# Performance work log

Measured on AMD Instinct MI355X. Metric: run time of the kernel, lower is better.

Reference implementation:

```python
import jax, jax.numpy as jnp
import numpy as np

DEPTH = 128
NEG_MAX = -jnp.finfo(jnp.float32).max


def setup_inputs() -> dict:
    key = jax.random.key(0)
    ks = jax.random.split(key, 10)
    B, S, F, C = 16, 2048, 512, 1000
    x = jax.random.normal(ks[0], (B, S, F), dtype=jnp.float32)
    attention_mask = jax.random.randint(ks[1], (B, S, S), 0, 2) == 1
    s = 1.0 / np.sqrt(F)
    Wq = jax.random.uniform(ks[2], (F, DEPTH), jnp.float32, -s, s)
    bq = jax.random.uniform(ks[3], (DEPTH,), jnp.float32, -s, s)
    Wk = jax.random.uniform(ks[4], (F, DEPTH), jnp.float32, -s, s)
    bk = jax.random.uniform(ks[5], (DEPTH,), jnp.float32, -s, s)
    Wv = jax.random.uniform(ks[6], (F, DEPTH), jnp.float32, -s, s)
    bv = jax.random.uniform(ks[7], (DEPTH,), jnp.float32, -s, s)
    sl = 1.0 / np.sqrt(DEPTH)
    Wl = jax.random.uniform(ks[8], (DEPTH, C), jnp.float32, -sl, sl)
    bl = jax.random.uniform(ks[9], (C,), jnp.float32, -sl, sl)
    return {"x": x, "attention_mask": attention_mask,
            "Wq": Wq, "bq": bq, "Wk": Wk, "bk": bk,
            "Wv": Wv, "bv": bv, "Wl": Wl, "bl": bl}


def reference(x, attention_mask, Wq, bq, Wk, bk, Wv, bv, Wl, bl):
    # x: [B, S, F]; single-head attention with depth=128
    q = (x @ Wq + bq) * (DEPTH ** -0.5)          # [B, S, D] (is_scaled_dot_product)
    k = x @ Wk + bk                               # [B, S, D]
    v = x @ Wv + bv                               # [B, S, D]
    logit = jnp.einsum('bsd,btd->bst', q, k)      # [B, S, S]
    # masked_fill_(mask, -float_max) then added to logits
    logit = logit + jnp.where(attention_mask, NEG_MAX, 0.0)
    attn = jax.nn.softmax(logit, axis=2)
    out = jnp.einsum('bst,btd->bsd', attn, v)     # [B, S, D]
    out = out @ Wl + bl                           # [B, S, C]
    return out.mean(axis=1)                       # [B, C]
```

## Files before the change

kernel.cpp:

```cpp
#include <hip/hip_runtime.h>
#include <stdint.h>

#define BB 16
#define SS 2048
#define FF 512
#define DD 128
#define CC 1000

typedef __attribute__((ext_vector_type(8))) short bf16x8;
typedef __attribute__((ext_vector_type(4))) float f32x4;

__device__ __forceinline__ unsigned short f2bf(float f) {
  unsigned x;
  __builtin_memcpy(&x, &f, 4);
  x = x + 0x7FFFu + ((x >> 16) & 1u);
  return (unsigned short)(x >> 16);
}
__device__ __forceinline__ float bf2f(unsigned short u) {
  unsigned x = ((unsigned)u) << 16;
  float f;
  __builtin_memcpy(&f, &x, 4);
  return f;
}
__device__ __forceinline__ unsigned pk2(float a, float b) {
  return (unsigned)f2bf(a) | ((unsigned)f2bf(b) << 16);
}

#define WS_PK   0
#define WS_Q    8388608
#define WS_K    16777216
#define WS_V    25165824
#define WS_WT   33554432
#define WS_WGP  33947648
#define WS_END  42336256

__global__ __launch_bounds__(256) void k_prep(const void* __restrict__ mask,
                                              const float* __restrict__ Wq,
                                              const float* __restrict__ Wk,
                                              const float* __restrict__ Wv,
                                              unsigned short* __restrict__ wt,
                                              unsigned* __restrict__ pk) {
  __shared__ unsigned red;
  const int tid = threadIdx.x;
  if (tid == 0) red = 0;
  __syncthreads();
  {
    unsigned a = 0;
    const unsigned* m32 = (const unsigned*)mask;
#pragma unroll
    for (int j = 0; j < 4; ++j) a |= m32[tid * 4 + j] & 0xFFFFFF00u;
    if (a) atomicOr(&red, 1u);
  }
  __syncthreads();
  const bool isInt = (red == 0);

  const long long base = (long long)blockIdx.x * 32768;
  for (int it = 0; it < 128; ++it) {
    long long e = base + it * 256 + tid;
    int val;
    if (isInt) val = ((const int*)mask)[e];
    else       val = ((const unsigned char*)mask)[e];
    unsigned long long bal = __ballot(val != 0);
    if ((tid & 31) == 0)
      pk[e >> 5] = (unsigned)((tid & 63) ? (bal >> 32) : bal);
  }

  if (blockIdx.x < 768) {
    int idx = blockIdx.x * 256 + tid;
    int ty = idx >> 16;
    int o = idx & 65535;
    int d = o >> 9, f = o & 511;
    const float* W = ty == 0 ? Wq : (ty == 1 ? Wk : Wv);
    wt[idx] = f2bf(W[f * DD + d]);
  }
}

__global__ __launch_bounds__(256) void k_proj(const float* __restrict__ xg,
                                              const unsigned short* __restrict__ wtg,
                                              const float* __restrict__ bq,
                                              const float* __restrict__ bk,
                                              const float* __restrict__ bv,
                                              unsigned short* __restrict__ qo,
                                              unsigned short* __restrict__ ko,
                                              unsigned short* __restrict__ vo) {
  __shared__ __align__(16) char lA[8192];
  __shared__ __align__(16) char lB[8192];
  const int tid = threadIdx.x;
  const int lane = tid & 63;
  const int wv = tid >> 6;
  const int colL = lane & 15, quad = lane >> 4;
  const int blk = blockIdx.x, ty = blockIdx.y;
  const float* bias = ty == 0 ? bq : (ty == 1 ? bk : bv);
  unsigned short* outp = ty == 0 ? qo : (ty == 1 ? ko : vo);
  const float scale = ty == 0 ? 0.08838834764831845f : 1.0f;
  const unsigned short* wbase = wtg + (size_t)ty * 65536;
  const int m0 = (wv & 1) * 64, n0 = (wv >> 1) * 64;

  f32x4 acc[4][4];
  const f32x4 z4 = {0.f, 0.f, 0.f, 0.f};
#pragma unroll
  for (int mi = 0; mi < 4; ++mi)
#pragma unroll
    for (int ni = 0; ni < 4; ++ni) acc[mi][ni] = z4;

  for (int ic = 0; ic < 16; ++ic) {
    const int k0 = ic * 32;
    uint4 va[2], vb[2];
#pragma unroll
    for (int rr = 0; rr < 2; ++rr) {
      int p = rr * 256 + tid;
      int row = p >> 2, c = p & 3;
      const float* xp = xg + (size_t)(blk * 128 + row) * FF + k0 + c * 8;
      float4 x0 = *(const float4*)xp;
      float4 x1 = *(const float4*)(xp + 4);
      va[rr].x = pk2(x0.x, x0.y); va[rr].y = pk2(x0.z, x0.w);
      va[rr].z = pk2(x1.x, x1.y); va[rr].w = pk2(x1.z, x1.w);
      vb[rr] = *(const uint4*)(wbase + (size_t)row * FF + k0 + c * 8);
    }
    __syncthreads();
#pragma unroll
    for (int rr = 0; rr < 2; ++rr) {
      int p = rr * 256 + tid;
      int row = p >> 2, c = p & 3;
      int phys = c ^ ((row >> 1) & 3);
      *(uint4*)(lA + row * 64 + phys * 16) = va[rr];
      *(uint4*)(lB + row * 64 + phys * 16) = vb[rr];
    }
    __syncthreads();
    bf16x8 af[4], bfr[4];
#pragma unroll
    for (int mi = 0; mi < 4; ++mi) {
      int ar = m0 + mi * 16 + colL;
      int phys = quad ^ ((ar >> 1) & 3);
      af[mi] = *(const bf16x8*)(lA + ar * 64 + phys * 16);
    }
#pragma unroll
    for (int ni = 0; ni < 4; ++ni) {
      int br = n0 + ni * 16 + colL;
      int phys = quad ^ ((br >> 1) & 3);
      bfr[ni] = *(const bf16x8*)(lB + br * 64 + phys * 16);
    }
#pragma unroll
    for (int mi = 0; mi < 4; ++mi)
#pragma unroll
      for (int ni = 0; ni < 4; ++ni)
        acc[mi][ni] = __builtin_amdgcn_mfma_f32_16x16x32_bf16(af[mi], bfr[ni], acc[mi][ni], 0, 0, 0);
  }
#pragma unroll
  for (int ni = 0; ni < 4; ++ni) {
    int col = n0 + ni * 16 + colL;
    float bval = bias[col];
#pragma unroll
    for (int mi = 0; mi < 4; ++mi) {
#pragma unroll
      for (int r = 0; r < 4; ++r) {
        int row = blk * 128 + m0 + mi * 16 + quad * 4 + r;
        float val = (acc[mi][ni][r] + bval) * scale;
        outp[(size_t)row * DD + col] = f2bf(val);
      }
    }
  }
}

__global__ __launch_bounds__(512, 2) void k_fatt(const unsigned short* __restrict__ qg,
                                                 const unsigned short* __restrict__ kg,
                                                 const unsigned* __restrict__ pk,
                                                 float* __restrict__ wgp) {
  extern __shared__ __align__(16) char smem[];
  unsigned short* pt = (unsigned short*)smem;
  char* kt = smem + 131072;
  unsigned* mk = (unsigned*)(smem + 147456);
  float* zfin = (float*)(smem + 155776);
  float* zinvl = (float*)(smem + 155904);

  const int tid = threadIdx.x;
  const int lane = tid & 63, wv = tid >> 6;
  const int colL = lane & 15, quad = lane >> 4;
  const int wr = wv & 1, wq = wv >> 1;
  const int r0 = blockIdx.x * 32;
  const int b = blockIdx.y;

  for (int i = tid; i < 2048; i += 512) {
    int row = i >> 6, w = i & 63;
    mk[row * 65 + w] = pk[((size_t)b * SS + r0 + row) * 64 + w];
  }
  if (tid < 32) zfin[tid] = 0.f;

  bf16x8 qf[4];
  {
    int qrow = r0 + wr * 16 + colL;
    const unsigned short* qp = qg + ((size_t)b * SS + qrow) * DD + quad * 8;
#pragma unroll
    for (int kk = 0; kk < 4; ++kk) qf[kk] = *(const bf16x8*)(qp + kk * 32);
  }

  const int krow = tid >> 3, kc8 = tid & 7;
  const unsigned short* kbase = kg + ((size_t)b * SS + krow) * DD;
  const int kswz0 = (kc8 ^ (krow & 7)) * 16;
  const int kswz1 = ((kc8 + 8) ^ (krow & 7)) * 16;

  uint4 kreg0 = *(const uint4*)(kbase + kc8 * 8);
  uint4 kreg1 = *(const uint4*)(kbase + kc8 * 8 + 64);
  *(uint4*)(kt + krow * 256 + kswz0) = kreg0;
  *(uint4*)(kt + krow * 256 + kswz1) = kreg1;
  __syncthreads();

  float z[4] = {0.f, 0.f, 0.f, 0.f};
  const int tb = wq * 16 + colL;

  for (int c = 0; c < 32; ++c) {
    if (c < 31) {
      const unsigned short* kb2 = kbase + (size_t)(c + 1) * 64 * DD;
      kreg0 = *(const uint4*)(kb2 + kc8 * 8);
      kreg1 = *(const uint4*)(kb2 + kc8 * 8 + 64);
    }
    bf16x8 bb[4];
#pragma unroll
    for (int kk = 0; kk < 4; ++kk) {
      int phys = (kk * 4 + quad) ^ (tb & 7);
      bb[kk] = *(const bf16x8*)(kt + tb * 256 + phys * 16);
    }
    f32x4 acc = {0.f, 0.f, 0.f, 0.f};
    acc = __builtin_amdgcn_mfma_f32_16x16x32_bf16(qf[0], bb[0], acc, 0, 0, 0);
    acc = __builtin_amdgcn_mfma_f32_16x16x32_bf16(qf[1], bb[1], acc, 0, 0, 0);
    acc = __builtin_amdgcn_mfma_f32_16x16x32_bf16(qf[2], bb[2], acc, 0, 0, 0);
    acc = __builtin_amdgcn_mfma_f32_16x16x32_bf16(qf[3], bb[3], acc, 0, 0, 0);
    int tl = c * 64 + tb;
    int widx = tl >> 5, wb = tl & 31;
#pragma unroll
    for (int r = 0; r < 4; ++r) {
      int row_l = wr * 16 + quad * 4 + r;
      unsigned mw = mk[row_l * 65 + widx];
      float e = ((mw >> wb) & 1u) ? 0.f : __expf(fminf(acc[r], 80.f));
      z[r] += e;
      pt[row_l * 2048 + (tl ^ ((row_l & 7) << 3))] = f2bf(e);
    }
    if (c < 31) {
      __syncthreads();
      *(uint4*)(kt + krow * 256 + kswz0) = kreg0;
      *(uint4*)(kt + krow * 256 + kswz1) = kreg1;
      __syncthreads();
    }
  }

#pragma unroll
  for (int r = 0; r < 4; ++r) {
    float s = z[r];
    s += __shfl_xor(s, 1, 64);
    s += __shfl_xor(s, 2, 64);
    s += __shfl_xor(s, 4, 64);
    s += __shfl_xor(s, 8, 64);
    if (colL == 0) atomicAdd(&zfin[wr * 16 + quad * 4 + r], s);
  }
  __syncthreads();
  if (tid < 32) zinvl[tid] = 1.0f / fmaxf(zfin[tid], 1e-30f);
  __syncthreads();

  {
    const int t0 = tid * 4;
    float a0 = 0.f, a1 = 0.f, a2 = 0.f, a3 = 0.f;
#pragma unroll 8
    for (int r = 0; r < 32; ++r) {
      const unsigned short* pr = pt + r * 2048 + (t0 ^ ((r & 7) << 3));
      ushort4 pv = *(const ushort4*)pr;
      float zi = zinvl[r];
      a0 += bf2f(pv.x) * zi;
      a1 += bf2f(pv.y) * zi;
      a2 += bf2f(pv.z) * zi;
      a3 += bf2f(pv.w) * zi;
    }
    float4 o4;
    o4.x = a0; o4.y = a1; o4.z = a2; o4.w = a3;
    *(float4*)(wgp + ((size_t)b * 64 + blockIdx.x) * SS + t0) = o4;
  }
}

__global__ __launch_bounds__(1024) void k_tail(const float* __restrict__ wgp,
                                               const unsigned short* __restrict__ vg,
                                               const float* __restrict__ Wl,
                                               const float* __restrict__ bl,
                                               float* __restrict__ outp) {
  __shared__ float ws2[2048];
  __shared__ float yp[8][128];
  __shared__ float ys[128];
  const int tid = threadIdx.x;
  const int b = blockIdx.x;

  {
    float s0 = 0.f, s1 = 0.f;
    const float* wp = wgp + ((size_t)b * 64) * SS + tid * 2;
#pragma unroll 8
    for (int rg = 0; rg < 64; ++rg) {
      s0 += wp[rg * SS];
      s1 += wp[rg * SS + 1];
    }
    ws2[tid * 2] = s0;
    ws2[tid * 2 + 1] = s1;
  }
  __syncthreads();

  {
    const int d = tid & 127, tg = tid >> 7;
    const int t0 = tg * 256;
    float p = 0.f;
    const unsigned short* vr = vg + ((size_t)b * SS + t0) * DD + d;
#pragma unroll 8
    for (int t = 0; t < 256; ++t) p += ws2[t0 + t] * bf2f(vr[(size_t)t * DD]);
    yp[tg][d] = p;
  }
  __syncthreads();
  if (tid < 128) {
    float a = 0.f;
#pragma unroll
    for (int g = 0; g < 8; ++g) a += yp[g][tid];
    ys[tid] = a * (1.0f / 2048.0f);
  }
  __syncthreads();

  if (tid < CC) {
    float a = bl[tid];
#pragma unroll 16
    for (int dd = 0; dd < DD; ++dd) a += ys[dd] * Wl[dd * CC + tid];
    outp[b * CC + tid] = a;
  }
}

extern "C" void kernel_launch(void* const* d_in, const int* in_sizes, int n_in,
                              void* d_out, int out_size, void* d_ws, size_t ws_size,
                              hipStream_t stream) {
  const void* ptr[10];
  for (int i = 0; i < 10; ++i) ptr[i] = (i < n_in) ? d_in[i] : nullptr;
  if (n_in == 10) {
    const void *px = 0, *pm = 0, *pWl = 0, *pbl = 0;
    const void* pW[3] = {0, 0, 0};
    const void* pb[3] = {0, 0, 0};
    int nW = 0, nb = 0;
    for (int i = 0; i < 10; ++i) {
      int s = in_sizes[i];
      if (s == 16777216) px = d_in[i];
      else if (s == 67108864) pm = d_in[i];
      else if (s == 128000) pWl = d_in[i];
      else if (s == 1000) pbl = d_in[i];
      else if (s == 65536 && nW < 3) pW[nW++] = d_in[i];
      else if (s == 128 && nb < 3) pb[nb++] = d_in[i];
    }
    if (px && pm && pWl && pbl && nW == 3 && nb == 3) {
      ptr[0] = px; ptr[1] = pm;
      ptr[2] = pW[0]; ptr[3] = pb[0];
      ptr[4] = pW[1]; ptr[5] = pb[1];
      ptr[6] = pW[2]; ptr[7] = pb[2];
      ptr[8] = pWl; ptr[9] = pbl;
    }
  }
  char* ws = (char*)d_ws;
  if (ws_size < (size_t)WS_END) return;
  unsigned* pk = (unsigned*)(ws + WS_PK);
  unsigned short* q  = (unsigned short*)(ws + WS_Q);
  unsigned short* k  = (unsigned short*)(ws + WS_K);
  unsigned short* v  = (unsigned short*)(ws + WS_V);
  unsigned short* wt = (unsigned short*)(ws + WS_WT);
  float* wgp = (float*)(ws + WS_WGP);

  k_prep<<<2048, 256, 0, stream>>>(ptr[1], (const float*)ptr[2], (const float*)ptr[4],
                                   (const float*)ptr[6], wt, pk);
  k_proj<<<dim3(256, 3), 256, 0, stream>>>((const float*)ptr[0], wt,
                                           (const float*)ptr[3], (const float*)ptr[5],
                                           (const float*)ptr[7], q, k, v);
  k_fatt<<<dim3(64, 16), 512, 156032, stream>>>(q, k, pk, wgp);
  k_tail<<<16, 1024, 0, stream>>>(wgp, v, (const float*)ptr[8], (const float*)ptr[9],
                                  (float*)d_out);
}
```

Measured before the change: 577.3 us.

## Halve query rows per attention block and read K directly from global memory

The attention kernel now handles 16 query rows per block instead of 32, which halves the shared-memory probability tile and doubles the grid to 128x16 blocks. The shared-memory K staging and its two per-chunk barriers are removed; each wave loads K fragments straight from global memory into double-buffered registers. This aims for more resident blocks per CU and less synchronisation. The cost is that every block re-reads all of K, with more redundant global/L2 traffic, and the tail kernel must sum twice as many partial rows.

```diff
diff --git a/kernel.cpp b/kernel.cpp
--- a/kernel.cpp
+++ b/kernel.cpp
@@ -32,7 +32,7 @@
 #define WS_V    25165824
 #define WS_WT   33554432
 #define WS_WGP  33947648
-#define WS_END  42336256
+#define WS_END  50724864
 
 __global__ __launch_bounds__(256) void k_prep(const void* __restrict__ mask,
                                               const float* __restrict__ Wq,
@@ -162,84 +162,69 @@
   }
 }
 
-__global__ __launch_bounds__(512, 2) void k_fatt(const unsigned short* __restrict__ qg,
+__global__ __launch_bounds__(512, 4) void k_fatt(const unsigned short* __restrict__ qg,
                                                  const unsigned short* __restrict__ kg,
                                                  const unsigned* __restrict__ pk,
                                                  float* __restrict__ wgp) {
-  extern __shared__ __align__(16) char smem[];
-  unsigned short* pt = (unsigned short*)smem;
-  char* kt = smem + 131072;
-  unsigned* mk = (unsigned*)(smem + 147456);
-  float* zfin = (float*)(smem + 155776);
-  float* zinvl = (float*)(smem + 155904);
+  __shared__ __align__(16) unsigned short pt[16 * 2048];
+  __shared__ unsigned mk[16 * 65];
+  __shared__ float zfin[16];
+  __shared__ float zinvl[16];
 
   const int tid = threadIdx.x;
-  const int lane = tid & 63, wv = tid >> 6;
+  const int lane = tid & 63, wq = tid >> 6;
   const int colL = lane & 15, quad = lane >> 4;
-  const int wr = wv & 1, wq = wv >> 1;
-  const int r0 = blockIdx.x * 32;
+  const int r0 = blockIdx.x * 16;
   const int b = blockIdx.y;
 
-  for (int i = tid; i < 2048; i += 512) {
+  for (int i = tid; i < 1024; i += 512) {
     int row = i >> 6, w = i & 63;
     mk[row * 65 + w] = pk[((size_t)b * SS + r0 + row) * 64 + w];
   }
-  if (tid < 32) zfin[tid] = 0.f;
+  if (tid < 16) zfin[tid] = 0.f;
 
   bf16x8 qf[4];
   {
-    int qrow = r0 + wr * 16 + colL;
+    int qrow = r0 + colL;
     const unsigned short* qp = qg + ((size_t)b * SS + qrow) * DD + quad * 8;
 #pragma unroll
     for (int kk = 0; kk < 4; ++kk) qf[kk] = *(const bf16x8*)(qp + kk * 32);
   }
-
-  const int krow = tid >> 3, kc8 = tid & 7;
-  const unsigned short* kbase = kg + ((size_t)b * SS + krow) * DD;
-  const int kswz0 = (kc8 ^ (krow & 7)) * 16;
-  const int kswz1 = ((kc8 + 8) ^ (krow & 7)) * 16;
-
-  uint4 kreg0 = *(const uint4*)(kbase + kc8 * 8);
-  uint4 kreg1 = *(const uint4*)(kbase + kc8 * 8 + 64);
-  *(uint4*)(kt + krow * 256 + kswz0) = kreg0;
-  *(uint4*)(kt + krow * 256 + kswz1) = kreg1;
-  __syncthreads();
-
+  __syncthreads();
+
+  const int rbase = quad * 4;
+  const unsigned short* kgb = kg + (size_t)b * SS * DD + quad * 8;
   float z[4] = {0.f, 0.f, 0.f, 0.f};
-  const int tb = wq * 16 + colL;
-
-  for (int c = 0; c < 32; ++c) {
-    if (c < 31) {
-      const unsigned short* kb2 = kbase + (size_t)(c + 1) * 64 * DD;
-      kreg0 = *(const uint4*)(kb2 + kc8 * 8);
-      kreg1 = *(const uint4*)(kb2 + kc8 * 8 + 64);
-    }
-    bf16x8 bb[4];
-#pragma unroll
-    for (int kk = 0; kk < 4; ++kk) {
-      int phys = (kk * 4 + quad) ^ (tb & 7);
-      bb[kk] = *(const bf16x8*)(kt + tb * 256 + phys * 16);
+
+  bf16x8 bb[2][4];
+  {
+    const unsigned short* kp = kgb + (size_t)(wq * 64 + colL) * DD;
+#pragma unroll
+    for (int kk = 0; kk < 4; ++kk) bb[0][kk] = *(const bf16x8*)(kp + kk * 32);
+  }
+#pragma unroll
+  for (int i = 0; i < 16; ++i) {
+    if (i < 15) {
+      const int i2 = i + 1;
+      const int t2 = (wq + 8 * (i2 >> 2)) * 64 + (i2 & 3) * 16 + colL;
+      const unsigned short* kp = kgb + (size_t)t2 * DD;
+#pragma unroll
+      for (int kk = 0; kk < 4; ++kk) bb[i2 & 1][kk] = *(const bf16x8*)(kp + kk * 32);
     }
     f32x4 acc = {0.f, 0.f, 0.f, 0.f};
-    acc = __builtin_amdgcn_mfma_f32_16x16x32_bf16(qf[0], bb[0], acc, 0, 0, 0);
-    acc = __builtin_amdgcn_mfma_f32_16x16x32_bf16(qf[1], bb[1], acc, 0, 0, 0);
-    acc = __builtin_amdgcn_mfma_f32_16x16x32_bf16(qf[2], bb[2], acc, 0, 0, 0);
-    acc = __builtin_amdgcn_mfma_f32_16x16x32_bf16(qf[3], bb[3], acc, 0, 0, 0);
-    int tl = c * 64 + tb;
-    int widx = tl >> 5, wb = tl & 31;
+    acc = __builtin_amdgcn_mfma_f32_16x16x32_bf16(qf[0], bb[i & 1][0], acc, 0, 0, 0);
+    acc = __builtin_amdgcn_mfma_f32_16x16x32_bf16(qf[1], bb[i & 1][1], acc, 0, 0, 0);
+    acc = __builtin_amdgcn_mfma_f32_16x16x32_bf16(qf[2], bb[i & 1][2], acc, 0, 0, 0);
+    acc = __builtin_amdgcn_mfma_f32_16x16x32_bf16(qf[3], bb[i & 1][3], acc, 0, 0, 0);
+    const int tl = (wq + 8 * (i >> 2)) * 64 + (i & 3) * 16 + colL;
+    const int widx = tl >> 5, wb = tl & 31;
 #pragma unroll
     for (int r = 0; r < 4; ++r) {
-      int row_l = wr * 16 + quad * 4 + r;
+      int row_l = rbase + r;
       unsigned mw = mk[row_l * 65 + widx];
       float e = ((mw >> wb) & 1u) ? 0.f : __expf(fminf(acc[r], 80.f));
       z[r] += e;
       pt[row_l * 2048 + (tl ^ ((row_l & 7) << 3))] = f2bf(e);
-    }
-    if (c < 31) {
-      __syncthreads();
-      *(uint4*)(kt + krow * 256 + kswz0) = kreg0;
-      *(uint4*)(kt + krow * 256 + kswz1) = kreg1;
-      __syncthreads();
     }
   }
 
@@ -250,17 +235,17 @@
     s += __shfl_xor(s, 2, 64);
     s += __shfl_xor(s, 4, 64);
     s += __shfl_xor(s, 8, 64);
-    if (colL == 0) atomicAdd(&zfin[wr * 16 + quad * 4 + r], s);
-  }
-  __syncthreads();
-  if (tid < 32) zinvl[tid] = 1.0f / fmaxf(zfin[tid], 1e-30f);
+    if (colL == 0) atomicAdd(&zfin[rbase + r], s);
+  }
+  __syncthreads();
+  if (tid < 16) zinvl[tid] = 1.0f / fmaxf(zfin[tid], 1e-30f);
   __syncthreads();
 
   {
     const int t0 = tid * 4;
     float a0 = 0.f, a1 = 0.f, a2 = 0.f, a3 = 0.f;
-#pragma unroll 8
-    for (int r = 0; r < 32; ++r) {
+#pragma unroll
+    for (int r = 0; r < 16; ++r) {
       const unsigned short* pr = pt + r * 2048 + (t0 ^ ((r & 7) << 3));
       ushort4 pv = *(const ushort4*)pr;
       float zi = zinvl[r];
@@ -271,7 +256,7 @@
     }
     float4 o4;
     o4.x = a0; o4.y = a1; o4.z = a2; o4.w = a3;
-    *(float4*)(wgp + ((size_t)b * 64 + blockIdx.x) * SS + t0) = o4;
+    *(float4*)(wgp + ((size_t)b * 128 + blockIdx.x) * SS + t0) = o4;
   }
 }
 
@@ -288,11 +273,11 @@
 
   {
     float s0 = 0.f, s1 = 0.f;
-    const float* wp = wgp + ((size_t)b * 64) * SS + tid * 2;
+    const float* wp = wgp + ((size_t)b * 128) * SS + tid * 2;
 #pragma unroll 8
-    for (int rg = 0; rg < 64; ++rg) {
-      s0 += wp[rg * SS];
-      s1 += wp[rg * SS + 1];
+    for (int rg = 0; rg < 128; ++rg) {
+      s0 += wp[(size_t)rg * SS];
+      s1 += wp[(size_t)rg * SS + 1];
     }
     ws2[tid * 2] = s0;
     ws2[tid * 2 + 1] = s1;
@@ -366,7 +351,7 @@
   k_proj<<<dim3(256, 3), 256, 0, stream>>>((const float*)ptr[0], wt,
                                            (const float*)ptr[3], (const float*)ptr[5],
                                            (const float*)ptr[7], q, k, v);
-  k_fatt<<<dim3(64, 16), 512, 156032, stream>>>(q, k, pk, wgp);
+  k_fatt<<<dim3(128, 16), 512, 0, stream>>>(q, k, pk, wgp);
   k_tail<<<16, 1024, 0, stream>>>(wgp, v, (const float*)ptr[8], (const float*)ptr[9],
                                   (float*)d_out);
 }
```

Result: slower. 629.4 us (+9.0%).
